# Kernel optimization log

Hardware: AMD Instinct MI355X
Metric: run time of the kernel (lower is better)

## Reference

```python
import jax, jax.numpy as jnp
import numpy as np

NUM_EXPERTS = 16
TOP_K = 4
N_GROUP = 4
TOPK_GROUP = 2
SCALING = 2.5


def setup_inputs() -> dict:
    key = jax.random.key(0)
    ks = jax.random.split(key, 9)
    B, S, H, I = 2, 1024, 2048, 1024
    w = lambda k, shape: jax.random.normal(k, shape, jnp.float32) * 0.02
    return {
        "hidden_states": jax.random.normal(ks[0], (B, S, H), jnp.float32),
        "gate_weight": w(ks[1], (NUM_EXPERTS, H)),
        "expert_bias": jnp.zeros((NUM_EXPERTS,), jnp.float32),
        "gate_proj": w(ks[2], (NUM_EXPERTS, I, H)),
        "up_proj": w(ks[3], (NUM_EXPERTS, I, H)),
        "down_proj": w(ks[4], (NUM_EXPERTS, H, I)),
        "shared_gate": w(ks[5], (I, H)),
        "shared_up": w(ks[6], (I, H)),
        "shared_down": w(ks[7], (H, I)),
    }


def _route(x, gate_weight, expert_bias):
    # x: [T, H] -> routing weights [T, K], selected experts [T, K]
    logits = x @ gate_weight.T                              # [T, E]
    scores = jax.nn.sigmoid(logits)
    biased = scores + expert_bias[None, :]                  # bias only for selection
    T = x.shape[0]
    gsz = NUM_EXPERTS // N_GROUP
    grp = biased.reshape(T, N_GROUP, gsz)
    top2, _ = jax.lax.top_k(grp, 2)
    group_scores = top2.sum(-1)                             # [T, G]
    _, gidx = jax.lax.top_k(group_scores, TOPK_GROUP)       # [T, topk_group]
    gmask = jax.nn.one_hot(gidx, N_GROUP, dtype=scores.dtype).sum(1)  # [T, G]
    emask = jnp.repeat(gmask, gsz, axis=1)                  # [T, E]
    masked = jnp.where(emask > 0, biased, -jnp.inf)
    _, sel = jax.lax.top_k(masked, TOP_K)                   # [T, K]
    w = jnp.take_along_axis(scores, sel, axis=1)            # weights from unbiased scores
    w = w / (w.sum(-1, keepdims=True) + 1e-20)              # norm_topk_prob
    return w * SCALING, sel


def _moe(x, w, sel, gate_proj, up_proj, down_proj):
    # combine weight per (token, expert): [T, E]; zero where expert not selected
    cw = (jax.nn.one_hot(sel, NUM_EXPERTS, dtype=x.dtype) * w[..., None]).sum(1)

    def body(acc, inp):
        g, u, d, we = inp                                   # g,u: [I,H]; d: [H,I]; we: [T]
        y = (jax.nn.silu(x @ g.T) * (x @ u.T)) @ d.T        # SwiGLU expert FFN
        return acc + we[:, None] * y, None

    out, _ = jax.lax.scan(body, jnp.zeros_like(x),
                          (gate_proj, up_proj, down_proj, cw.T))
    return out


def reference(hidden_states, gate_weight, expert_bias, gate_proj, up_proj,
              down_proj, shared_gate, shared_up, shared_down):
    B, S, H = hidden_states.shape
    x = hidden_states.reshape(-1, H)                        # [T, H]
    w, sel = _route(x, gate_weight, expert_bias)
    out = _moe(x, w, sel, gate_proj, up_proj, down_proj)
    shared = (jax.nn.silu(x @ shared_gate.T) * (x @ shared_up.T)) @ shared_down.T
    return (out + shared).reshape(B, S, H)
```

## Files before the change

kernel.cpp:

```cpp
#include <hip/hip_runtime.h>
#include <hip/hip_bf16.h>
#include <stdint.h>

#define T_TOK 2048
#define HDIM  2048
#define IDIM  1024
#define NEXP  16
#define SCALING 2.5f

typedef __attribute__((ext_vector_type(8))) short bf16x8;
typedef __attribute__((ext_vector_type(4))) float f32x4;

static __device__ __forceinline__ unsigned short f2bf(float f) {
    uint32_t u = __float_as_uint(f);
    u += 0x7FFF + ((u >> 16) & 1);
    return (unsigned short)(u >> 16);
}

#define GLD_LDS16(g, l) \
    __builtin_amdgcn_global_load_lds((const __attribute__((address_space(1))) uint32_t*)(g), \
                                     (__attribute__((address_space(3))) uint32_t*)(l), 16, 0, 0)

__global__ __launch_bounds__(256) void cvtw_k(const float* __restrict__ gate_w,
                                              const float* __restrict__ up_w,
                                              const float* __restrict__ shg,
                                              const float* __restrict__ shu,
                                              const float* __restrict__ down_w,
                                              const float* __restrict__ shd,
                                              unsigned short* __restrict__ wbf1,
                                              unsigned short* __restrict__ wbf2) {
    int b = blockIdx.x;
    const float* src;
    unsigned short* dst;
    size_t flat;
    if (b < 34816) {
        flat = ((size_t)b * 256 + threadIdx.x) * 8;
        int e   = (int)(flat >> 22);
        int rem = (int)(flat & ((1u << 22) - 1));
        int row = rem >> 11;
        int h   = rem & 2047;
        int f   = row >> 1;
        if (e == NEXP) src = (row & 1) ? shu : shg;
        else           src = ((row & 1) ? up_w : gate_w) + (size_t)e * (IDIM * HDIM);
        src += (size_t)f * HDIM + h;
        dst = wbf1 + flat;
    } else {
        flat = ((size_t)(b - 34816) * 256 + threadIdx.x) * 8;
        int e   = (int)(flat >> 21);
        int rem = (int)(flat & ((1u << 21) - 1));
        src = ((e == NEXP) ? shd : (down_w + (size_t)e * (HDIM * IDIM))) + rem;
        dst = wbf2 + flat;
    }
    float4 f0 = *(const float4*)src;
    float4 f1 = *(const float4*)(src + 4);
    union { unsigned short s[8]; uint4 v; } u;
    u.s[0] = f2bf(f0.x); u.s[1] = f2bf(f0.y); u.s[2] = f2bf(f0.z); u.s[3] = f2bf(f0.w);
    u.s[4] = f2bf(f1.x); u.s[5] = f2bf(f1.y); u.s[6] = f2bf(f1.z); u.s[7] = f2bf(f1.w);
    *(uint4*)dst = u.v;
}

__global__ __launch_bounds__(256) void route2_k(const float* __restrict__ x,
                                                const float* __restrict__ gw,
                                                const float* __restrict__ bias,
                                                unsigned short* __restrict__ Xbf,
                                                int* __restrict__ tokl,
                                                float* __restrict__ twl,
                                                int* __restrict__ cnt,
                                                int* __restrict__ sl4) {
    __shared__ float sx[HDIM];
    __shared__ float slog[NEXP];
    int t = blockIdx.x;
    int tid = threadIdx.x;
    const float* xp = x + (size_t)t * HDIM;
    float4 f0 = *(const float4*)(xp + tid * 8);
    float4 f1 = *(const float4*)(xp + tid * 8 + 4);
    union { unsigned short h[8]; uint4 v; } u;
    u.h[0] = f2bf(f0.x); u.h[1] = f2bf(f0.y); u.h[2] = f2bf(f0.z); u.h[3] = f2bf(f0.w);
    u.h[4] = f2bf(f1.x); u.h[5] = f2bf(f1.y); u.h[6] = f2bf(f1.z); u.h[7] = f2bf(f1.w);
    *(uint4*)(Xbf + (size_t)t * HDIM + tid * 8) = u.v;
    *(float4*)(sx + tid * 8) = f0;
    *(float4*)(sx + tid * 8 + 4) = f1;
    __syncthreads();
    int e = tid >> 4, r = tid & 15;
    const float* wp = gw + (size_t)e * HDIM;
    float p = 0.f;
    for (int j = r; j < HDIM; j += 16) p += sx[j] * wp[j];
    for (int off = 8; off; off >>= 1) p += __shfl_down(p, off, 16);
    if (r == 0) slog[e] = p;
    __syncthreads();
    if (tid == 0) {
        float sc[NEXP], bi[NEXP];
        for (int i = 0; i < NEXP; i++) {
            sc[i] = 1.f / (1.f + expf(-slog[i]));
            bi[i] = sc[i] + bias[i];
        }
        float gsc[4];
        for (int g = 0; g < 4; g++) {
            float v0 = bi[g*4+0], v1 = bi[g*4+1], v2 = bi[g*4+2], v3 = bi[g*4+3];
            float hi01 = fmaxf(v0, v1), lo01 = fminf(v0, v1);
            float hi23 = fmaxf(v2, v3), lo23 = fminf(v2, v3);
            float top1 = fmaxf(hi01, hi23);
            float sec  = fmaxf(fminf(hi01, hi23), (hi01 >= hi23) ? lo01 : lo23);
            gsc[g] = top1 + sec;
        }
        int g0 = 0; for (int g = 1; g < 4; g++) if (gsc[g] > gsc[g0]) g0 = g;
        int g1 = (g0 == 0) ? 1 : 0;
        for (int g = 0; g < 4; g++) if (g != g0 && gsc[g] > gsc[g1]) g1 = g;
        float mk[NEXP];
        for (int i = 0; i < NEXP; i++) {
            int gg = i >> 2;
            mk[i] = (gg == g0 || gg == g1) ? bi[i] : -INFINITY;
        }
        int sel[4]; float wv[4]; float wsum = 0.f;
        for (int k = 0; k < 4; k++) {
            int bmax = 0; float bv = -INFINITY;
            for (int i = 0; i < NEXP; i++) if (mk[i] > bv) { bv = mk[i]; bmax = i; }
            sel[k] = bmax; mk[bmax] = -INFINITY;
            wv[k] = sc[bmax]; wsum += sc[bmax];
        }
        float scale = SCALING / (wsum + 1e-20f);
        for (int k = 0; k < 4; k++) {
            int ee = sel[k];
            int slot = atomicAdd(&cnt[ee], 1);
            tokl[ee * T_TOK + slot] = t;
            twl[ee * T_TOK + slot] = wv[k] * scale;
            sl4[t * 4 + k] = ee * T_TOK + slot;
        }
    }
}

__global__ __launch_bounds__(512, 2) void gemm1_k(const unsigned short* __restrict__ Xbf,
                                                  const unsigned short* __restrict__ wbf1,
                                                  const int* __restrict__ tokl,
                                                  const int* __restrict__ cnt,
                                                  unsigned short* __restrict__ act) {
    extern __shared__ unsigned short sm[];
    int b = blockIdx.x;
    int swz = (b & 7) * 136 + (b >> 3);
    int e = swz >> 6, mt = (swz >> 3) & 7, nt = swz & 7;
    int C = (e == NEXP) ? T_TOK : cnt[e];
    int m0 = mt * 256;
    if (m0 >= C) return;
    int tid = threadIdx.x;

    int c8 = tid & 7, rr = tid >> 3;
    int swzc = c8 ^ (rr & 7);
    const char* aA[4];
    const char* aB[4];
#pragma unroll
    for (int i = 0; i < 4; i++) {
        int slot = m0 + i * 64 + rr;
        int sl = (slot < C) ? slot : (C - 1);
        int tk = (e == NEXP) ? sl : tokl[e * T_TOK + sl];
        aA[i] = (const char*)Xbf + ((size_t)tk * HDIM + (size_t)swzc * 8) * 2;
        int brow = nt * 256 + i * 64 + rr;
        aB[i] = (const char*)wbf1 + (((size_t)e << 22) + (size_t)brow * HDIM + (size_t)swzc * 8) * 2;
    }

    int lane = tid & 63, wid = tid >> 6;
    int wm = wid >> 2, wn = wid & 3;
    int fr = lane & 15, kg = lane >> 4;
    int xo = fr & 7;

    f32x4 acc[8][4];
#pragma unroll
    for (int m = 0; m < 8; m++)
#pragma unroll
        for (int n = 0; n < 4; n++) acc[m][n] = (f32x4){0.f, 0.f, 0.f, 0.f};

    auto stage = [&](int kt, int bf) {
        size_t kb = (size_t)kt * 128;
        char* dA = (char*)(sm + bf * 16384);
        char* dB = (char*)(sm + 32768 + bf * 16384);
#pragma unroll
        for (int i = 0; i < 4; i++) GLD_LDS16(aA[i] + kb, dA + i * 8192 + tid * 16);
#pragma unroll
        for (int i = 0; i < 4; i++) GLD_LDS16(aB[i] + kb, dB + i * 8192 + tid * 16);
    };

    stage(0, 0);
    asm volatile("s_waitcnt vmcnt(0)" ::: "memory");
    __builtin_amdgcn_s_barrier();

    const int NT = 32;
    for (int kt = 0; kt < NT; ++kt) {
        int bf = kt & 1;
        __builtin_amdgcn_s_barrier();
        __builtin_amdgcn_sched_barrier(0);
        if (kt + 1 < NT) {
            stage(kt + 1, bf ^ 1);
            asm volatile("s_waitcnt vmcnt(8)" ::: "memory");
        } else {
            asm volatile("s_waitcnt vmcnt(0)" ::: "memory");
        }
        __builtin_amdgcn_s_barrier();
        __builtin_amdgcn_sched_barrier(0);

        const char* lA = (const char*)(sm + bf * 16384);
        const char* lB = (const char*)(sm + 32768 + bf * 16384);
        bf16x8 bv[4][2];
#pragma unroll
        for (int n = 0; n < 4; n++)
#pragma unroll
            for (int h = 0; h < 2; h++)
                bv[n][h] = *(const bf16x8*)(lB + (wn * 64 + n * 16 + fr) * 128 + ((((h << 2) | kg) ^ xo) << 4));
#pragma unroll
        for (int p = 0; p < 4; p++) {
            bf16x8 av[2][2];
#pragma unroll
            for (int mm = 0; mm < 2; mm++)
#pragma unroll
                for (int h = 0; h < 2; h++)
                    av[mm][h] = *(const bf16x8*)(lA + (wm * 128 + (p * 2 + mm) * 16 + fr) * 128 + ((((h << 2) | kg) ^ xo) << 4));
            asm volatile("s_waitcnt lgkmcnt(0)" ::: "memory");
            __builtin_amdgcn_sched_barrier(0);
            __builtin_amdgcn_s_setprio(1);
#pragma unroll
            for (int h = 0; h < 2; h++)
#pragma unroll
                for (int n = 0; n < 4; n++) {
                    acc[p * 2 + 0][n] = __builtin_amdgcn_mfma_f32_16x16x32_bf16(av[0][h], bv[n][h], acc[p * 2 + 0][n], 0, 0, 0);
                    acc[p * 2 + 1][n] = __builtin_amdgcn_mfma_f32_16x16x32_bf16(av[1][h], bv[n][h], acc[p * 2 + 1][n], 0, 0, 0);
                }
            __builtin_amdgcn_s_setprio(0);
        }
    }

    unsigned short* actE = act + (size_t)e * T_TOK * IDIM;
#pragma unroll
    for (int m = 0; m < 8; m++)
#pragma unroll
        for (int n = 0; n < 4; n++)
#pragma unroll
            for (int q = 0; q < 4; q++) {
                float v = acc[m][n][q];
                float pu = __shfl_xor(v, 1, 64);
                int slot = m0 + wm * 128 + m * 16 + kg * 4 + q;
                if (!(lane & 1) && slot < C) {
                    float g = v, u2 = pu;
                    float a = g / (1.f + __expf(-g)) * u2;
                    int j = nt * 128 + wn * 32 + n * 8 + (fr >> 1);
                    actE[(size_t)slot * IDIM + j] = f2bf(a);
                }
            }
}

__global__ __launch_bounds__(512, 2) void gemm2_k(const unsigned short* __restrict__ act,
                                                  const unsigned short* __restrict__ wbf2,
                                                  const float* __restrict__ twl,
                                                  const int* __restrict__ cnt,
                                                  unsigned short* __restrict__ part) {
    extern __shared__ unsigned short sm[];
    int b = blockIdx.x;
    int swz = (b & 7) * 136 + (b >> 3);
    int e = swz >> 6, mt = (swz >> 3) & 7, nt = swz & 7;
    int C = (e == NEXP) ? T_TOK : cnt[e];
    int m0 = mt * 256;
    if (m0 >= C) return;
    int nb = nt * 256;
    int tid = threadIdx.x;

    const unsigned short* actE = act + (size_t)e * T_TOK * IDIM;
    int c8 = tid & 7, rr = tid >> 3;
    int swzc = c8 ^ (rr & 7);
    const char* aA[4];
    const char* aB[4];
#pragma unroll
    for (int i = 0; i < 4; i++) {
        int slot = m0 + i * 64 + rr;
        aA[i] = (const char*)actE + ((size_t)slot * IDIM + (size_t)swzc * 8) * 2;
        aB[i] = (const char*)wbf2 + (((size_t)e << 21) + (size_t)(nb + i * 64 + rr) * IDIM + (size_t)swzc * 8) * 2;
    }

    int lane = tid & 63, wid = tid >> 6;
    int wm = wid >> 2, wn = wid & 3;
    int fr = lane & 15, kg = lane >> 4;
    int xo = fr & 7;

    f32x4 acc[8][4];
#pragma unroll
    for (int m = 0; m < 8; m++)
#pragma unroll
        for (int n = 0; n < 4; n++) acc[m][n] = (f32x4){0.f, 0.f, 0.f, 0.f};

    auto stage = [&](int kt, int bf) {
        size_t kb = (size_t)kt * 128;
        char* dA = (char*)(sm + bf * 16384);
        char* dB = (char*)(sm + 32768 + bf * 16384);
#pragma unroll
        for (int i = 0; i < 4; i++) GLD_LDS16(aA[i] + kb, dA + i * 8192 + tid * 16);
#pragma unroll
        for (int i = 0; i < 4; i++) GLD_LDS16(aB[i] + kb, dB + i * 8192 + tid * 16);
    };

    stage(0, 0);
    asm volatile("s_waitcnt vmcnt(0)" ::: "memory");
    __builtin_amdgcn_s_barrier();

    const int NT = 16;
    for (int kt = 0; kt < NT; ++kt) {
        int bf = kt & 1;
        __builtin_amdgcn_s_barrier();
        __builtin_amdgcn_sched_barrier(0);
        if (kt + 1 < NT) {
            stage(kt + 1, bf ^ 1);
            asm volatile("s_waitcnt vmcnt(8)" ::: "memory");
        } else {
            asm volatile("s_waitcnt vmcnt(0)" ::: "memory");
        }
        __builtin_amdgcn_s_barrier();
        __builtin_amdgcn_sched_barrier(0);

        const char* lA = (const char*)(sm + bf * 16384);
        const char* lB = (const char*)(sm + 32768 + bf * 16384);
        bf16x8 bv[4][2];
#pragma unroll
        for (int n = 0; n < 4; n++)
#pragma unroll
            for (int h = 0; h < 2; h++)
                bv[n][h] = *(const bf16x8*)(lB + (wn * 64 + n * 16 + fr) * 128 + ((((h << 2) | kg) ^ xo) << 4));
#pragma unroll
        for (int p = 0; p < 4; p++) {
            bf16x8 av[2][2];
#pragma unroll
            for (int mm = 0; mm < 2; mm++)
#pragma unroll
                for (int h = 0; h < 2; h++)
                    av[mm][h] = *(const bf16x8*)(lA + (wm * 128 + (p * 2 + mm) * 16 + fr) * 128 + ((((h << 2) | kg) ^ xo) << 4));
            asm volatile("s_waitcnt lgkmcnt(0)" ::: "memory");
            __builtin_amdgcn_sched_barrier(0);
            __builtin_amdgcn_s_setprio(1);
#pragma unroll
            for (int h = 0; h < 2; h++)
#pragma unroll
                for (int n = 0; n < 4; n++) {
                    acc[p * 2 + 0][n] = __builtin_amdgcn_mfma_f32_16x16x32_bf16(av[0][h], bv[n][h], acc[p * 2 + 0][n], 0, 0, 0);
                    acc[p * 2 + 1][n] = __builtin_amdgcn_mfma_f32_16x16x32_bf16(av[1][h], bv[n][h], acc[p * 2 + 1][n], 0, 0, 0);
                }
            __builtin_amdgcn_s_setprio(0);
        }
    }

#pragma unroll
    for (int m = 0; m < 8; m++)
#pragma unroll
        for (int q = 0; q < 4; q++) {
            int slot = m0 + wm * 128 + m * 16 + kg * 4 + q;
            if (slot >= C) continue;
            float wg = (e == NEXP) ? 1.f : twl[e * T_TOK + slot];
            unsigned short* pr = part + (size_t)(e * T_TOK + slot) * HDIM + nb + wn * 64 + fr;
#pragma unroll
            for (int n = 0; n < 4; n++)
                pr[n * 16] = f2bf(wg * acc[m][n][q]);
        }
}

__global__ __launch_bounds__(256) void reduce_k(const unsigned short* __restrict__ part,
                                                const int* __restrict__ sl4,
                                                float* __restrict__ out) {
    int t = blockIdx.x;
    int h = threadIdx.x * 8;
    int4 s = *(const int4*)(sl4 + t * 4);
    const unsigned short* p0 = part + (size_t)s.x * HDIM + h;
    const unsigned short* p1 = part + (size_t)s.y * HDIM + h;
    const unsigned short* p2 = part + (size_t)s.z * HDIM + h;
    const unsigned short* p3 = part + (size_t)s.w * HDIM + h;
    const unsigned short* p4 = part + (size_t)(NEXP * T_TOK + t) * HDIM + h;
    float o[8];
#pragma unroll
    for (int i = 0; i < 8; i++) o[i] = 0.f;
    auto addv = [&](const unsigned short* p) {
        uint4 a = *(const uint4*)p;
        const unsigned short* q = (const unsigned short*)&a;
#pragma unroll
        for (int i = 0; i < 8; i++) o[i] += __uint_as_float((uint32_t)q[i] << 16);
    };
    addv(p0); addv(p1); addv(p2); addv(p3); addv(p4);
    float4 r0 = {o[0], o[1], o[2], o[3]};
    float4 r1 = {o[4], o[5], o[6], o[7]};
    *(float4*)(out + (size_t)t * HDIM + h) = r0;
    *(float4*)(out + (size_t)t * HDIM + h + 4) = r1;
}

extern "C" void kernel_launch(void* const* d_in, const int* in_sizes, int n_in,
                              void* d_out, int out_size, void* d_ws, size_t ws_size,
                              hipStream_t stream) {
    const float* x      = (const float*)d_in[0];
    const float* gw     = (const float*)d_in[1];
    const float* bias   = (const float*)d_in[2];
    const float* gate_w = (const float*)d_in[3];
    const float* up_w   = (const float*)d_in[4];
    const float* down_w = (const float*)d_in[5];
    const float* shg    = (const float*)d_in[6];
    const float* shu    = (const float*)d_in[7];
    const float* shd    = (const float*)d_in[8];
    float* out = (float*)d_out;
    char* ws = (char*)d_ws;

    unsigned short* Xbf  = (unsigned short*)ws;
    unsigned short* act  = (unsigned short*)(ws + 8388608ULL);
    unsigned short* wbf1 = (unsigned short*)(ws + 79691776ULL);
    unsigned short* wbf2 = (unsigned short*)(ws + 222298112ULL);
    int*            tokl = (int*)(ws + 293601280ULL);
    float*          twl  = (float*)(ws + 293732352ULL);
    int*            cnt  = (int*)(ws + 293863424ULL);
    int*            sl4  = (int*)(ws + 293863488ULL);
    unsigned short* part = wbf1;

    static bool attr_set = false;
    if (!attr_set) {
        hipFuncSetAttribute((const void*)gemm1_k, hipFuncAttributeMaxDynamicSharedMemorySize, 131072);
        hipFuncSetAttribute((const void*)gemm2_k, hipFuncAttributeMaxDynamicSharedMemorySize, 131072);
        attr_set = true;
    }

    hipMemsetAsync(cnt, 0, 64, stream);
    cvtw_k<<<52224, 256, 0, stream>>>(gate_w, up_w, shg, shu, down_w, shd, wbf1, wbf2);
    route2_k<<<2048, 256, 0, stream>>>(x, gw, bias, Xbf, tokl, twl, cnt, sl4);
    gemm1_k<<<1088, 512, 131072, stream>>>(Xbf, wbf1, tokl, cnt, act);
    gemm2_k<<<1088, 512, 131072, stream>>>(act, wbf2, twl, cnt, part);
    reduce_k<<<2048, 256, 0, stream>>>(part, sl4, out);
}
```

Baseline: 843.9 us.

## Halve GEMM M-tile to 128 rows and fuse weight conversion with routing

```diff
diff --git a/kernel.cpp b/kernel.cpp
--- a/kernel.cpp
+++ b/kernel.cpp
@@ -21,56 +21,57 @@
     __builtin_amdgcn_global_load_lds((const __attribute__((address_space(1))) uint32_t*)(g), \
                                      (__attribute__((address_space(3))) uint32_t*)(l), 16, 0, 0)
 
-__global__ __launch_bounds__(256) void cvtw_k(const float* __restrict__ gate_w,
-                                              const float* __restrict__ up_w,
-                                              const float* __restrict__ shg,
-                                              const float* __restrict__ shu,
-                                              const float* __restrict__ down_w,
-                                              const float* __restrict__ shd,
-                                              unsigned short* __restrict__ wbf1,
-                                              unsigned short* __restrict__ wbf2) {
-    int b = blockIdx.x;
-    const float* src;
-    unsigned short* dst;
-    size_t flat;
-    if (b < 34816) {
-        flat = ((size_t)b * 256 + threadIdx.x) * 8;
-        int e   = (int)(flat >> 22);
-        int rem = (int)(flat & ((1u << 22) - 1));
-        int row = rem >> 11;
-        int h   = rem & 2047;
-        int f   = row >> 1;
-        if (e == NEXP) src = (row & 1) ? shu : shg;
-        else           src = ((row & 1) ? up_w : gate_w) + (size_t)e * (IDIM * HDIM);
-        src += (size_t)f * HDIM + h;
-        dst = wbf1 + flat;
-    } else {
-        flat = ((size_t)(b - 34816) * 256 + threadIdx.x) * 8;
-        int e   = (int)(flat >> 21);
-        int rem = (int)(flat & ((1u << 21) - 1));
-        src = ((e == NEXP) ? shd : (down_w + (size_t)e * (HDIM * IDIM))) + rem;
-        dst = wbf2 + flat;
-    }
-    float4 f0 = *(const float4*)src;
-    float4 f1 = *(const float4*)(src + 4);
-    union { unsigned short s[8]; uint4 v; } u;
-    u.s[0] = f2bf(f0.x); u.s[1] = f2bf(f0.y); u.s[2] = f2bf(f0.z); u.s[3] = f2bf(f0.w);
-    u.s[4] = f2bf(f1.x); u.s[5] = f2bf(f1.y); u.s[6] = f2bf(f1.z); u.s[7] = f2bf(f1.w);
-    *(uint4*)dst = u.v;
-}
-
-__global__ __launch_bounds__(256) void route2_k(const float* __restrict__ x,
-                                                const float* __restrict__ gw,
-                                                const float* __restrict__ bias,
-                                                unsigned short* __restrict__ Xbf,
-                                                int* __restrict__ tokl,
-                                                float* __restrict__ twl,
-                                                int* __restrict__ cnt,
-                                                int* __restrict__ sl4) {
+__global__ __launch_bounds__(256) void cvtrt_k(const float* __restrict__ gate_w,
+                                               const float* __restrict__ up_w,
+                                               const float* __restrict__ shg,
+                                               const float* __restrict__ shu,
+                                               const float* __restrict__ down_w,
+                                               const float* __restrict__ shd,
+                                               const float* __restrict__ x,
+                                               const float* __restrict__ gw,
+                                               const float* __restrict__ bias,
+                                               unsigned short* __restrict__ wbf1,
+                                               unsigned short* __restrict__ wbf2,
+                                               unsigned short* __restrict__ Xbf,
+                                               int* __restrict__ tokl,
+                                               float* __restrict__ twl,
+                                               int* __restrict__ cnt,
+                                               int* __restrict__ sl4) {
     __shared__ float sx[HDIM];
     __shared__ float slog[NEXP];
-    int t = blockIdx.x;
+    int b = blockIdx.x;
     int tid = threadIdx.x;
+    if (b < 52224) {
+        const float* src;
+        unsigned short* dst;
+        size_t flat;
+        if (b < 34816) {
+            flat = ((size_t)b * 256 + tid) * 8;
+            int e   = (int)(flat >> 22);
+            int rem = (int)(flat & ((1u << 22) - 1));
+            int row = rem >> 11;
+            int h   = rem & 2047;
+            int f   = row >> 1;
+            if (e == NEXP) src = (row & 1) ? shu : shg;
+            else           src = ((row & 1) ? up_w : gate_w) + (size_t)e * (IDIM * HDIM);
+            src += (size_t)f * HDIM + h;
+            dst = wbf1 + flat;
+        } else {
+            flat = ((size_t)(b - 34816) * 256 + tid) * 8;
+            int e   = (int)(flat >> 21);
+            int rem = (int)(flat & ((1u << 21) - 1));
+            src = ((e == NEXP) ? shd : (down_w + (size_t)e * (HDIM * IDIM))) + rem;
+            dst = wbf2 + flat;
+        }
+        float4 f0 = *(const float4*)src;
+        float4 f1 = *(const float4*)(src + 4);
+        union { unsigned short s[8]; uint4 v; } u;
+        u.s[0] = f2bf(f0.x); u.s[1] = f2bf(f0.y); u.s[2] = f2bf(f0.z); u.s[3] = f2bf(f0.w);
+        u.s[4] = f2bf(f1.x); u.s[5] = f2bf(f1.y); u.s[6] = f2bf(f1.z); u.s[7] = f2bf(f1.w);
+        *(uint4*)dst = u.v;
+        return;
+    }
+    int t = b - 52224;
     const float* xp = x + (size_t)t * HDIM;
     float4 f0 = *(const float4*)(xp + tid * 8);
     float4 f1 = *(const float4*)(xp + tid * 8 + 4);
@@ -136,23 +137,27 @@
                                                   unsigned short* __restrict__ act) {
     extern __shared__ unsigned short sm[];
     int b = blockIdx.x;
-    int swz = (b & 7) * 136 + (b >> 3);
-    int e = swz >> 6, mt = (swz >> 3) & 7, nt = swz & 7;
+    int swz = (b & 7) * 272 + (b >> 3);
+    int e = swz >> 7, rtile = swz & 127;
+    int nt = rtile >> 4, mt = rtile & 15;
     int C = (e == NEXP) ? T_TOK : cnt[e];
-    int m0 = mt * 256;
+    int m0 = mt * 128;
     if (m0 >= C) return;
     int tid = threadIdx.x;
 
     int c8 = tid & 7, rr = tid >> 3;
     int swzc = c8 ^ (rr & 7);
-    const char* aA[4];
+    const char* aA[2];
     const char* aB[4];
 #pragma unroll
-    for (int i = 0; i < 4; i++) {
+    for (int i = 0; i < 2; i++) {
         int slot = m0 + i * 64 + rr;
         int sl = (slot < C) ? slot : (C - 1);
         int tk = (e == NEXP) ? sl : tokl[e * T_TOK + sl];
         aA[i] = (const char*)Xbf + ((size_t)tk * HDIM + (size_t)swzc * 8) * 2;
+    }
+#pragma unroll
+    for (int i = 0; i < 4; i++) {
         int brow = nt * 256 + i * 64 + rr;
         aB[i] = (const char*)wbf1 + (((size_t)e << 22) + (size_t)brow * HDIM + (size_t)swzc * 8) * 2;
     }
@@ -162,18 +167,18 @@
     int fr = lane & 15, kg = lane >> 4;
     int xo = fr & 7;
 
-    f32x4 acc[8][4];
-#pragma unroll
-    for (int m = 0; m < 8; m++)
+    f32x4 acc[4][4];
+#pragma unroll
+    for (int m = 0; m < 4; m++)
 #pragma unroll
         for (int n = 0; n < 4; n++) acc[m][n] = (f32x4){0.f, 0.f, 0.f, 0.f};
 
     auto stage = [&](int kt, int bf) {
         size_t kb = (size_t)kt * 128;
-        char* dA = (char*)(sm + bf * 16384);
-        char* dB = (char*)(sm + 32768 + bf * 16384);
-#pragma unroll
-        for (int i = 0; i < 4; i++) GLD_LDS16(aA[i] + kb, dA + i * 8192 + tid * 16);
+        char* dA = (char*)sm + bf * 16384;
+        char* dB = (char*)sm + 32768 + bf * 32768;
+#pragma unroll
+        for (int i = 0; i < 2; i++) GLD_LDS16(aA[i] + kb, dA + i * 8192 + tid * 16);
 #pragma unroll
         for (int i = 0; i < 4; i++) GLD_LDS16(aB[i] + kb, dB + i * 8192 + tid * 16);
     };
@@ -189,15 +194,15 @@
         __builtin_amdgcn_sched_barrier(0);
         if (kt + 1 < NT) {
             stage(kt + 1, bf ^ 1);
-            asm volatile("s_waitcnt vmcnt(8)" ::: "memory");
+            asm volatile("s_waitcnt vmcnt(6)" ::: "memory");
         } else {
             asm volatile("s_waitcnt vmcnt(0)" ::: "memory");
         }
         __builtin_amdgcn_s_barrier();
         __builtin_amdgcn_sched_barrier(0);
 
-        const char* lA = (const char*)(sm + bf * 16384);
-        const char* lB = (const char*)(sm + 32768 + bf * 16384);
+        const char* lA = (const char*)sm + bf * 16384;
+        const char* lB = (const char*)sm + 32768 + bf * 32768;
         bf16x8 bv[4][2];
 #pragma unroll
         for (int n = 0; n < 4; n++)
@@ -205,13 +210,13 @@
             for (int h = 0; h < 2; h++)
                 bv[n][h] = *(const bf16x8*)(lB + (wn * 64 + n * 16 + fr) * 128 + ((((h << 2) | kg) ^ xo) << 4));
 #pragma unroll
-        for (int p = 0; p < 4; p++) {
+        for (int p = 0; p < 2; p++) {
             bf16x8 av[2][2];
 #pragma unroll
             for (int mm = 0; mm < 2; mm++)
 #pragma unroll
                 for (int h = 0; h < 2; h++)
-                    av[mm][h] = *(const bf16x8*)(lA + (wm * 128 + (p * 2 + mm) * 16 + fr) * 128 + ((((h << 2) | kg) ^ xo) << 4));
+                    av[mm][h] = *(const bf16x8*)(lA + (wm * 64 + (p * 2 + mm) * 16 + fr) * 128 + ((((h << 2) | kg) ^ xo) << 4));
             asm volatile("s_waitcnt lgkmcnt(0)" ::: "memory");
             __builtin_amdgcn_sched_barrier(0);
             __builtin_amdgcn_s_setprio(1);
@@ -228,14 +233,14 @@
 
     unsigned short* actE = act + (size_t)e * T_TOK * IDIM;
 #pragma unroll
-    for (int m = 0; m < 8; m++)
+    for (int m = 0; m < 4; m++)
 #pragma unroll
         for (int n = 0; n < 4; n++)
 #pragma unroll
             for (int q = 0; q < 4; q++) {
                 float v = acc[m][n][q];
                 float pu = __shfl_xor(v, 1, 64);
-                int slot = m0 + wm * 128 + m * 16 + kg * 4 + q;
+                int slot = m0 + wm * 64 + m * 16 + kg * 4 + q;
                 if (!(lane & 1) && slot < C) {
                     float g = v, u2 = pu;
                     float a = g / (1.f + __expf(-g)) * u2;
@@ -252,10 +257,11 @@
                                                   unsigned short* __restrict__ part) {
     extern __shared__ unsigned short sm[];
     int b = blockIdx.x;
-    int swz = (b & 7) * 136 + (b >> 3);
-    int e = swz >> 6, mt = (swz >> 3) & 7, nt = swz & 7;
+    int swz = (b & 7) * 272 + (b >> 3);
+    int e = swz >> 7, rtile = swz & 127;
+    int nt = rtile >> 4, mt = rtile & 15;
     int C = (e == NEXP) ? T_TOK : cnt[e];
-    int m0 = mt * 256;
+    int m0 = mt * 128;
     if (m0 >= C) return;
     int nb = nt * 256;
     int tid = threadIdx.x;
@@ -263,12 +269,15 @@
     const unsigned short* actE = act + (size_t)e * T_TOK * IDIM;
     int c8 = tid & 7, rr = tid >> 3;
     int swzc = c8 ^ (rr & 7);
-    const char* aA[4];
+    const char* aA[2];
     const char* aB[4];
 #pragma unroll
-    for (int i = 0; i < 4; i++) {
+    for (int i = 0; i < 2; i++) {
         int slot = m0 + i * 64 + rr;
         aA[i] = (const char*)actE + ((size_t)slot * IDIM + (size_t)swzc * 8) * 2;
+    }
+#pragma unroll
+    for (int i = 0; i < 4; i++) {
         aB[i] = (const char*)wbf2 + (((size_t)e << 21) + (size_t)(nb + i * 64 + rr) * IDIM + (size_t)swzc * 8) * 2;
     }
 
@@ -277,18 +286,18 @@
     int fr = lane & 15, kg = lane >> 4;
     int xo = fr & 7;
 
-    f32x4 acc[8][4];
-#pragma unroll
-    for (int m = 0; m < 8; m++)
+    f32x4 acc[4][4];
+#pragma unroll
+    for (int m = 0; m < 4; m++)
 #pragma unroll
         for (int n = 0; n < 4; n++) acc[m][n] = (f32x4){0.f, 0.f, 0.f, 0.f};
 
     auto stage = [&](int kt, int bf) {
         size_t kb = (size_t)kt * 128;
-        char* dA = (char*)(sm + bf * 16384);
-        char* dB = (char*)(sm + 32768 + bf * 16384);
-#pragma unroll
-        for (int i = 0; i < 4; i++) GLD_LDS16(aA[i] + kb, dA + i * 8192 + tid * 16);
+        char* dA = (char*)sm + bf * 16384;
+        char* dB = (char*)sm + 32768 + bf * 32768;
+#pragma unroll
+        for (int i = 0; i < 2; i++) GLD_LDS16(aA[i] + kb, dA + i * 8192 + tid * 16);
 #pragma unroll
         for (int i = 0; i < 4; i++) GLD_LDS16(aB[i] + kb, dB + i * 8192 + tid * 16);
     };
@@ -304,15 +313,15 @@
         __builtin_amdgcn_sched_barrier(0);
         if (kt + 1 < NT) {
             stage(kt + 1, bf ^ 1);
-            asm volatile("s_waitcnt vmcnt(8)" ::: "memory");
+            asm volatile("s_waitcnt vmcnt(6)" ::: "memory");
         } else {
             asm volatile("s_waitcnt vmcnt(0)" ::: "memory");
         }
         __builtin_amdgcn_s_barrier();
         __builtin_amdgcn_sched_barrier(0);
 
-        const char* lA = (const char*)(sm + bf * 16384);
-        const char* lB = (const char*)(sm + 32768 + bf * 16384);
+        const char* lA = (const char*)sm + bf * 16384;
+        const char* lB = (const char*)sm + 32768 + bf * 32768;
         bf16x8 bv[4][2];
 #pragma unroll
         for (int n = 0; n < 4; n++)
@@ -320,13 +329,13 @@
             for (int h = 0; h < 2; h++)
                 bv[n][h] = *(const bf16x8*)(lB + (wn * 64 + n * 16 + fr) * 128 + ((((h << 2) | kg) ^ xo) << 4));
 #pragma unroll
-        for (int p = 0; p < 4; p++) {
+        for (int p = 0; p < 2; p++) {
             bf16x8 av[2][2];
 #pragma unroll
             for (int mm = 0; mm < 2; mm++)
 #pragma unroll
                 for (int h = 0; h < 2; h++)
-                    av[mm][h] = *(const bf16x8*)(lA + (wm * 128 + (p * 2 + mm) * 16 + fr) * 128 + ((((h << 2) | kg) ^ xo) << 4));
+                    av[mm][h] = *(const bf16x8*)(lA + (wm * 64 + (p * 2 + mm) * 16 + fr) * 128 + ((((h << 2) | kg) ^ xo) << 4));
             asm volatile("s_waitcnt lgkmcnt(0)" ::: "memory");
             __builtin_amdgcn_sched_barrier(0);
             __builtin_amdgcn_s_setprio(1);
@@ -342,10 +351,10 @@
     }
 
 #pragma unroll
-    for (int m = 0; m < 8; m++)
+    for (int m = 0; m < 4; m++)
 #pragma unroll
         for (int q = 0; q < 4; q++) {
-            int slot = m0 + wm * 128 + m * 16 + kg * 4 + q;
+            int slot = m0 + wm * 64 + m * 16 + kg * 4 + q;
             if (slot >= C) continue;
             float wg = (e == NEXP) ? 1.f : twl[e * T_TOK + slot];
             unsigned short* pr = part + (size_t)(e * T_TOK + slot) * HDIM + nb + wn * 64 + fr;
@@ -409,15 +418,15 @@
 
     static bool attr_set = false;
     if (!attr_set) {
-        hipFuncSetAttribute((const void*)gemm1_k, hipFuncAttributeMaxDynamicSharedMemorySize, 131072);
-        hipFuncSetAttribute((const void*)gemm2_k, hipFuncAttributeMaxDynamicSharedMemorySize, 131072);
+        hipFuncSetAttribute((const void*)gemm1_k, hipFuncAttributeMaxDynamicSharedMemorySize, 98304);
+        hipFuncSetAttribute((const void*)gemm2_k, hipFuncAttributeMaxDynamicSharedMemorySize, 98304);
         attr_set = true;
     }
 
     hipMemsetAsync(cnt, 0, 64, stream);
-    cvtw_k<<<52224, 256, 0, stream>>>(gate_w, up_w, shg, shu, down_w, shd, wbf1, wbf2);
-    route2_k<<<2048, 256, 0, stream>>>(x, gw, bias, Xbf, tokl, twl, cnt, sl4);
-    gemm1_k<<<1088, 512, 131072, stream>>>(Xbf, wbf1, tokl, cnt, act);
-    gemm2_k<<<1088, 512, 131072, stream>>>(act, wbf2, twl, cnt, part);
+    cvtrt_k<<<54272, 256, 0, stream>>>(gate_w, up_w, shg, shu, down_w, shd,
+                                       x, gw, bias, wbf1, wbf2, Xbf, tokl, twl, cnt, sl4);
+    gemm1_k<<<2176, 512, 98304, stream>>>(Xbf, wbf1, tokl, cnt, act);
+    gemm2_k<<<2176, 512, 98304, stream>>>(act, wbf2, twl, cnt, part);
     reduce_k<<<2048, 256, 0, stream>>>(part, sl4, out);
 }
```

New measurement: 881.4 us. 1.04x slower.
